# Performance work log

Measured on AMD Instinct MI355X. Metric: run time of the kernel, lower is better.

The kernel has to match this reference:

```python
import jax, jax.numpy as jnp
import numpy as np

B, T, I = 32768, 28, 28
H, C = 128, 10


def setup_inputs() -> dict:
    key = jax.random.key(0)
    ks = jax.random.split(key, 7)
    s_u = 1.0 / np.sqrt(I)
    s_w = 1.0 / np.sqrt(H)
    return {
        "x": jax.random.normal(ks[0], (B, T, I), dtype=jnp.float32),
        "U_w": jax.random.uniform(ks[1], (H, I), jnp.float32, -s_u, s_u),
        "U_b": jax.random.uniform(ks[2], (H,), jnp.float32, -s_u, s_u),
        "W_w": jax.random.uniform(ks[3], (H, H), jnp.float32, -s_w, s_w),
        "W_b": jax.random.uniform(ks[4], (H,), jnp.float32, -s_w, s_w),
        "V_w": jax.random.uniform(ks[5], (C, H), jnp.float32, -s_w, s_w),
        "V_b": jax.random.uniform(ks[6], (C,), jnp.float32, -s_w, s_w),
    }


def reference(x, U_w, U_b, W_w, W_b, V_w, V_b):
    # x: [B, T, I]. Precompute input projections for all timesteps at once
    # (one big GEMM), then scan the sequential recurrence on S.
    ux = jnp.einsum("bti,hi->tbh", x, U_w) + U_b  # [T, B, H]

    def step(S, ux_t):
        S = jnp.tanh(ux_t + S @ W_w.T + W_b)
        return S, None

    S0 = jnp.zeros((x.shape[0], W_w.shape[0]), dtype=x.dtype)
    S_final, _ = jax.lax.scan(step, S0, ux)
    return S_final @ V_w.T + V_b  # [B, C]
```

## Files before the change

### kernel.cpp

```cpp
#include <hip/hip_runtime.h>


#define T_STEPS 28
#define S_STRIDE 132
#define X_STRIDE 900
#define XSLOTS 3136

typedef __attribute__((ext_vector_type(4))) float f32x4;
typedef __attribute__((ext_vector_type(8))) short short8;

#define MFMA16 __builtin_amdgcn_mfma_f32_16x16x32_bf16

__device__ __forceinline__ unsigned pack2(float lo, float hi) {
#if __has_builtin(__builtin_amdgcn_cvt_pk_bf16_f32)
  auto p = __builtin_amdgcn_cvt_pk_bf16_f32(lo, hi);
  return __builtin_bit_cast(unsigned, p);
#else
  unsigned a = __builtin_bit_cast(unsigned, lo);
  a += 0x7FFFu + ((a >> 16) & 1u);
  unsigned b = __builtin_bit_cast(unsigned, hi);
  b += 0x7FFFu + ((b >> 16) & 1u);
  return (a >> 16) | (b & 0xFFFF0000u);
#endif
}

__device__ __forceinline__ float bf2f(unsigned short s) {
  return __builtin_bit_cast(float, (unsigned)s << 16);
}

__device__ __forceinline__ short8 to_frag(f32x4 a, f32x4 b) {
  union { unsigned u[4]; short8 v; } r;
  r.u[0] = pack2(a[0], a[1]);
  r.u[1] = pack2(a[2], a[3]);
  r.u[2] = pack2(b[0], b[1]);
  r.u[3] = pack2(b[2], b[3]);
  return r.v;
}

__device__ __forceinline__ short8 load_frag64(const unsigned short* sp, int off) {
  union { uint2 d[2]; short8 v; } r;
  r.d[0] = *(const uint2*)(sp + off);
  r.d[1] = *(const uint2*)(sp + off + 4);
  return r.v;
}

__device__ __forceinline__ f32x4 tanh4(f32x4 z) {
  f32x4 x2 = z * z;
  f32x4 p = 945.0f + x2 * (105.0f + x2);
  f32x4 q = 945.0f + x2 * (420.0f + 15.0f * x2);
  f32x4 num = z * p;
  f32x4 r;
#pragma unroll
  for (int i = 0; i < 4; ++i) r[i] = __builtin_amdgcn_rcpf(q[i]);
  f32x4 t = num * r;
#pragma unroll
  for (int i = 0; i < 4; ++i) t[i] = __builtin_amdgcn_fmed3f(t[i], -1.0f, 1.0f);
  return t;
}

__global__ __launch_bounds__(256, 4) void rnn_fused(
    const float* __restrict__ x,  const float* __restrict__ Uw,
    const float* __restrict__ Ub, const float* __restrict__ Ww,
    const float* __restrict__ Wb, const float* __restrict__ Vw,
    const float* __restrict__ Vb, float* __restrict__ out) {
  __shared__ __align__(16) unsigned short Sbuf[2][16 * S_STRIDE];
  __shared__ __align__(16) unsigned short Xbuf[16 * X_STRIDE];

  const int tid  = threadIdx.x;
  const int w    = tid >> 6;
  const int lane = tid & 63;
  const int l15  = lane & 15;
  const int q    = lane >> 4;
  const int mrow = w * 32;
  const int b0   = blockIdx.x * 16;

  const f32x4 zero4 = {0.f, 0.f, 0.f, 0.f};
  const float* xblk = x + (size_t)b0 * 784;

  {
    f32x4 xr[13];
#pragma unroll
    for (int k = 0; k < 13; ++k) {
      int s = tid + 256 * k;
      if (s < XSLOTS) xr[k] = *(const f32x4*)(xblk + s * 4);
    }
#pragma unroll
    for (int k = 0; k < 13; ++k) {
      int s = tid + 256 * k;
      if (s < XSLOTS) {
        int row = s / 196, g = s - row * 196, tt = g / 7, j = g - tt * 7;
        uint2 d; d.x = pack2(xr[k][0], xr[k][1]); d.y = pack2(xr[k][2], xr[k][3]);
        *(uint2*)(Xbuf + row * X_STRIDE + tt * 32 + j * 4) = d;
        if (j == 0) {
          uint2 zz; zz.x = 0u; zz.y = 0u;
          *(uint2*)(Xbuf + row * X_STRIDE + tt * 32 + 28) = zz;
        }
      }
    }
  }

  short8 wfrag[2][4];
  short8 ufrag[2];
  f32x4  bias[2];
#pragma unroll
  for (int mt = 0; mt < 2; ++mt) {
    const int h = mrow + mt * 16 + l15;
    const float* wp = Ww + h * 128 + q * 8;
#pragma unroll
    for (int kt = 0; kt < 4; ++kt) {
      wfrag[mt][kt] = to_frag(*(const f32x4*)wp, *(const f32x4*)(wp + 4));
      wp += 32;
    }
    const float* up = Uw + h * 28 + q * 8;
    f32x4 u0 = *(const f32x4*)up;
    f32x4 u1 = zero4;
    if (q < 3) u1 = *(const f32x4*)(up + 4);
    ufrag[mt] = to_frag(u0, u1);
    const int hb = mrow + mt * 16 + q * 4;
    bias[mt] = *(const f32x4*)(Wb + hb) + *(const f32x4*)(Ub + hb);
  }
  __syncthreads();

  const int ro = l15 * S_STRIDE;
  const int xo = l15 * X_STRIDE + q * 8;
  f32x4 acc[2];

  {
    short8 xf = load_frag64(&Xbuf[0], xo);
    unsigned short* wp = &Sbuf[1][0];
#pragma unroll
    for (int mt = 0; mt < 2; ++mt) {
      f32x4 d0 = MFMA16(ufrag[mt], xf, bias[mt], 0, 0, 0);
      f32x4 t0 = tanh4(d0);
      uint2 dd; dd.x = pack2(t0[0], t0[1]); dd.y = pack2(t0[2], t0[3]);
      *(uint2*)(wp + ro + mrow + mt * 16 + q * 4) = dd;
    }
  }
  __syncthreads();

#pragma unroll 1
  for (int t = 1; t < T_STEPS; ++t) {
    short8 xf = load_frag64(&Xbuf[0], xo + t * 32);

    const unsigned short* sp = &Sbuf[t & 1][0] + ro + q * 8;

    short8 sA = load_frag64(sp, 0);
#pragma unroll
    for (int mt = 0; mt < 2; ++mt)
      acc[mt] = MFMA16(wfrag[mt][0], sA, bias[mt], 0, 0, 0);
#pragma unroll
    for (int kt = 1; kt < 4; ++kt) {
      sA = load_frag64(sp, kt * 32);
#pragma unroll
      for (int mt = 0; mt < 2; ++mt)
        acc[mt] = MFMA16(wfrag[mt][kt], sA, acc[mt], 0, 0, 0);
    }
#pragma unroll
    for (int mt = 0; mt < 2; ++mt)
      acc[mt] = MFMA16(ufrag[mt], xf, acc[mt], 0, 0, 0);

    unsigned short* wp = &Sbuf[(t + 1) & 1][0];
#pragma unroll
    for (int mt = 0; mt < 2; ++mt) {
      f32x4 th = tanh4(acc[mt]);
      uint2 dd; dd.x = pack2(th[0], th[1]); dd.y = pack2(th[2], th[3]);
      *(uint2*)(wp + ro + mrow + mt * 16 + q * 4) = dd;
    }
    __syncthreads();
  }

  {
    const int r  = tid >> 4;
    const int c0 = tid & 15;
    if (c0 < 10) {
      const float* v0 = Vw + c0 * 128;
      const unsigned short* srow = &Sbuf[0][0] + r * S_STRIDE;
      float a0 = 0.f;
#pragma unroll 8
      for (int h = 0; h < 128; ++h) a0 += bf2f(srow[h]) * v0[h];
      out[(size_t)(b0 + r) * 10 + c0] = a0 + Vb[c0];
    }
  }
}

extern "C" void kernel_launch(void* const* d_in, const int* in_sizes, int n_in,
                              void* d_out, int out_size, void* d_ws, size_t ws_size,
                              hipStream_t stream) {
  const float* x  = (const float*)d_in[0];
  const float* Uw = (const float*)d_in[1];
  const float* Ub = (const float*)d_in[2];
  const float* Ww = (const float*)d_in[3];
  const float* Wb = (const float*)d_in[4];
  const float* Vw = (const float*)d_in[5];
  const float* Vb = (const float*)d_in[6];
  rnn_fused<<<2048, 256, 0, stream>>>(x, Uw, Ub, Ww, Wb, Vw, Vb, (float*)d_out);
}
```

Measured before the change: 202.9 us.

## Give each wavefront its own batch tile and drop block-wide barriers

Each wavefront now owns a 16-row batch tile and computes all 128 hidden units, holding the full W and U matrices as bf16 fragments in registers. This removes the per-step __syncthreads, because state exchange happens only within the wave through a private XOR-swizzled LDS double buffer. The x input is streamed from global memory one timestep ahead instead of being staged whole into LDS. The grid drops to 512 blocks and launch bounds are relaxed. The cost is far higher register pressure (32 W fragments per lane) and lower occupancy, with possible spills.

```diff
diff --git a/kernel.cpp b/kernel.cpp
--- a/kernel.cpp
+++ b/kernel.cpp
@@ -2,9 +2,6 @@
 
 
 #define T_STEPS 28
-#define S_STRIDE 132
-#define X_STRIDE 900
-#define XSLOTS 3136
 
 typedef __attribute__((ext_vector_type(4))) float f32x4;
 typedef __attribute__((ext_vector_type(8))) short short8;
@@ -24,23 +21,12 @@
 #endif
 }
 
-__device__ __forceinline__ float bf2f(unsigned short s) {
-  return __builtin_bit_cast(float, (unsigned)s << 16);
-}
-
 __device__ __forceinline__ short8 to_frag(f32x4 a, f32x4 b) {
   union { unsigned u[4]; short8 v; } r;
   r.u[0] = pack2(a[0], a[1]);
   r.u[1] = pack2(a[2], a[3]);
   r.u[2] = pack2(b[0], b[1]);
   r.u[3] = pack2(b[2], b[3]);
-  return r.v;
-}
-
-__device__ __forceinline__ short8 load_frag64(const unsigned short* sp, int off) {
-  union { uint2 d[2]; short8 v; } r;
-  r.d[0] = *(const uint2*)(sp + off);
-  r.d[1] = *(const uint2*)(sp + off + 4);
   return r.v;
 }
 
@@ -58,127 +44,119 @@
   return t;
 }
 
-__global__ __launch_bounds__(256, 4) void rnn_fused(
+__global__ __launch_bounds__(256) void rnn_fused(
     const float* __restrict__ x,  const float* __restrict__ Uw,
     const float* __restrict__ Ub, const float* __restrict__ Ww,
     const float* __restrict__ Wb, const float* __restrict__ Vw,
     const float* __restrict__ Vb, float* __restrict__ out) {
-  __shared__ __align__(16) unsigned short Sbuf[2][16 * S_STRIDE];
-  __shared__ __align__(16) unsigned short Xbuf[16 * X_STRIDE];
+  __shared__ __align__(16) char lds[4 * 2 * 16 * 256];
 
   const int tid  = threadIdx.x;
   const int w    = tid >> 6;
   const int lane = tid & 63;
   const int l15  = lane & 15;
   const int q    = lane >> 4;
-  const int mrow = w * 32;
-  const int b0   = blockIdx.x * 16;
+  const int bw   = (blockIdx.x * 4 + w) * 16;
 
+  char* WB       = lds + (w << 13);
+  const int rowb = l15 << 8;
+  const int swz  = (l15 & 7) << 4;
   const f32x4 zero4 = {0.f, 0.f, 0.f, 0.f};
-  const float* xblk = x + (size_t)b0 * 784;
+
+  const float* xp = x + (size_t)(bw + l15) * 784 + q * 8;
+
+  f32x4 xa = *(const f32x4*)xp;
+  f32x4 xb = zero4;
+  if (q < 3) xb = *(const f32x4*)(xp + 4);
+
+  short8 wfrag[8][4];
+  short8 ufrag[8];
+  f32x4  bias[8];
+#pragma unroll
+  for (int mt = 0; mt < 8; ++mt) {
+    const int h = mt * 16 + l15;
+    const float* wp = Ww + h * 128 + q * 8;
+#pragma unroll
+    for (int kt = 0; kt < 4; ++kt)
+      wfrag[mt][kt] =
+          to_frag(*(const f32x4*)(wp + kt * 32), *(const f32x4*)(wp + kt * 32 + 4));
+    const float* up = Uw + h * 28 + q * 8;
+    f32x4 u1 = zero4;
+    if (q < 3) u1 = *(const f32x4*)(up + 4);
+    ufrag[mt] = to_frag(*(const f32x4*)up, u1);
+    const int hb = mt * 16 + q * 4;
+    bias[mt] = *(const f32x4*)(Wb + hb) + *(const f32x4*)(Ub + hb);
+  }
 
   {
-    f32x4 xr[13];
+    short8 xf = to_frag(xa, xb);
+    const float* xn = xp + 28;
+    xa = *(const f32x4*)xn;
+    xb = zero4;
+    if (q < 3) xb = *(const f32x4*)(xn + 4);
 #pragma unroll
-    for (int k = 0; k < 13; ++k) {
-      int s = tid + 256 * k;
-      if (s < XSLOTS) xr[k] = *(const f32x4*)(xblk + s * 4);
+    for (int mt = 0; mt < 8; ++mt) {
+      f32x4 d  = MFMA16(ufrag[mt], xf, bias[mt], 0, 0, 0);
+      f32x4 th = tanh4(d);
+      uint2 dd; dd.x = pack2(th[0], th[1]); dd.y = pack2(th[2], th[3]);
+      *(uint2*)(WB + rowb + ((mt * 32 + q * 8) ^ swz)) = dd;
     }
+  }
+
+  const float* xn = xp + 56;
+#pragma unroll 1
+  for (int t = 1; t < T_STEPS; ++t) {
+    short8 xf = to_frag(xa, xb);
+    if (t < T_STEPS - 1) {
+      xa = *(const f32x4*)xn;
+      if (q < 3) xb = *(const f32x4*)(xn + 4); else xb = zero4;
+      xn += 28;
+    }
+    const char* rbuf = WB + (((t & 1) ^ 1) << 12);
+    char*       wbuf = WB + ((t & 1) << 12);
+
+    short8 sfrag[4];
 #pragma unroll
-    for (int k = 0; k < 13; ++k) {
-      int s = tid + 256 * k;
-      if (s < XSLOTS) {
-        int row = s / 196, g = s - row * 196, tt = g / 7, j = g - tt * 7;
-        uint2 d; d.x = pack2(xr[k][0], xr[k][1]); d.y = pack2(xr[k][2], xr[k][3]);
-        *(uint2*)(Xbuf + row * X_STRIDE + tt * 32 + j * 4) = d;
-        if (j == 0) {
-          uint2 zz; zz.x = 0u; zz.y = 0u;
-          *(uint2*)(Xbuf + row * X_STRIDE + tt * 32 + 28) = zz;
-        }
+    for (int kt = 0; kt < 4; ++kt)
+      sfrag[kt] = *(const short8*)(rbuf + rowb + ((kt * 64 + q * 16) ^ swz));
+
+#pragma unroll
+    for (int g = 0; g < 2; ++g) {
+      f32x4 acc[4];
+#pragma unroll
+      for (int i = 0; i < 4; ++i)
+        acc[i] = MFMA16(ufrag[g * 4 + i], xf, bias[g * 4 + i], 0, 0, 0);
+#pragma unroll
+      for (int kt = 0; kt < 4; ++kt)
+#pragma unroll
+        for (int i = 0; i < 4; ++i)
+          acc[i] = MFMA16(wfrag[g * 4 + i][kt], sfrag[kt], acc[i], 0, 0, 0);
+#pragma unroll
+      for (int i = 0; i < 4; ++i) {
+        f32x4 th = tanh4(acc[i]);
+        const int mt = g * 4 + i;
+        uint2 dd; dd.x = pack2(th[0], th[1]); dd.y = pack2(th[2], th[3]);
+        *(uint2*)(wbuf + rowb + ((mt * 32 + q * 8) ^ swz)) = dd;
       }
     }
   }
 
-  short8 wfrag[2][4];
-  short8 ufrag[2];
-  f32x4  bias[2];
+  {
+    const char* sb   = WB + (((T_STEPS - 1) & 1) << 12);
+    const int   br   = lane & 15;
+    const int   c0   = lane >> 4;
+    const char* srow = sb + (br << 8);
+    const int   sw   = (br & 7) << 4;
+    for (int c = c0; c < 10; c += 4) {
+      const float* vp = Vw + c * 128;
+      float a0 = Vb[c];
 #pragma unroll
-  for (int mt = 0; mt < 2; ++mt) {
-    const int h = mrow + mt * 16 + l15;
-    const float* wp = Ww + h * 128 + q * 8;
-#pragma unroll
-    for (int kt = 0; kt < 4; ++kt) {
-      wfrag[mt][kt] = to_frag(*(const f32x4*)wp, *(const f32x4*)(wp + 4));
-      wp += 32;
-    }
-    const float* up = Uw + h * 28 + q * 8;
-    f32x4 u0 = *(const f32x4*)up;
-    f32x4 u1 = zero4;
-    if (q < 3) u1 = *(const f32x4*)(up + 4);
-    ufrag[mt] = to_frag(u0, u1);
-    const int hb = mrow + mt * 16 + q * 4;
-    bias[mt] = *(const f32x4*)(Wb + hb) + *(const f32x4*)(Ub + hb);
-  }
-  __syncthreads();
-
-  const int ro = l15 * S_STRIDE;
-  const int xo = l15 * X_STRIDE + q * 8;
-  f32x4 acc[2];
-
-  {
-    short8 xf = load_frag64(&Xbuf[0], xo);
-    unsigned short* wp = &Sbuf[1][0];
-#pragma unroll
-    for (int mt = 0; mt < 2; ++mt) {
-      f32x4 d0 = MFMA16(ufrag[mt], xf, bias[mt], 0, 0, 0);
-      f32x4 t0 = tanh4(d0);
-      uint2 dd; dd.x = pack2(t0[0], t0[1]); dd.y = pack2(t0[2], t0[3]);
-      *(uint2*)(wp + ro + mrow + mt * 16 + q * 4) = dd;
-    }
-  }
-  __syncthreads();
-
-#pragma unroll 1
-  for (int t = 1; t < T_STEPS; ++t) {
-    short8 xf = load_frag64(&Xbuf[0], xo + t * 32);
-
-    const unsigned short* sp = &Sbuf[t & 1][0] + ro + q * 8;
-
-    short8 sA = load_frag64(sp, 0);
-#pragma unroll
-    for (int mt = 0; mt < 2; ++mt)
-      acc[mt] = MFMA16(wfrag[mt][0], sA, bias[mt], 0, 0, 0);
-#pragma unroll
-    for (int kt = 1; kt < 4; ++kt) {
-      sA = load_frag64(sp, kt * 32);
-#pragma unroll
-      for (int mt = 0; mt < 2; ++mt)
-        acc[mt] = MFMA16(wfrag[mt][kt], sA, acc[mt], 0, 0, 0);
-    }
-#pragma unroll
-    for (int mt = 0; mt < 2; ++mt)
-      acc[mt] = MFMA16(ufrag[mt], xf, acc[mt], 0, 0, 0);
-
-    unsigned short* wp = &Sbuf[(t + 1) & 1][0];
-#pragma unroll
-    for (int mt = 0; mt < 2; ++mt) {
-      f32x4 th = tanh4(acc[mt]);
-      uint2 dd; dd.x = pack2(th[0], th[1]); dd.y = pack2(th[2], th[3]);
-      *(uint2*)(wp + ro + mrow + mt * 16 + q * 4) = dd;
-    }
-    __syncthreads();
-  }
-
-  {
-    const int r  = tid >> 4;
-    const int c0 = tid & 15;
-    if (c0 < 10) {
-      const float* v0 = Vw + c0 * 128;
-      const unsigned short* srow = &Sbuf[0][0] + r * S_STRIDE;
-      float a0 = 0.f;
-#pragma unroll 8
-      for (int h = 0; h < 128; ++h) a0 += bf2f(srow[h]) * v0[h];
-      out[(size_t)(b0 + r) * 10 + c0] = a0 + Vb[c0];
+      for (int hh = 0; hh < 128; hh += 2) {
+        unsigned d = *(const unsigned*)(srow + ((hh * 2) ^ sw));
+        a0 += __builtin_bit_cast(float, d << 16) * vp[hh];
+        a0 += __builtin_bit_cast(float, d & 0xFFFF0000u) * vp[hh + 1];
+      }
+      out[(size_t)(bw + br) * 10 + c] = a0;
     }
   }
 }
@@ -193,5 +171,5 @@
   const float* Wb = (const float*)d_in[4];
   const float* Vw = (const float*)d_in[5];
   const float* Vb = (const float*)d_in[6];
-  rnn_fused<<<2048, 256, 0, stream>>>(x, Uw, Ub, Ww, Wb, Vw, Vb, (float*)d_out);
+  rnn_fused<<<512, 256, 0, stream>>>(x, Uw, Ub, Ww, Wb, Vw, Vb, (float*)d_out);
 }
```

After: 245.1 us. +20.8%, slower.

## Stream x per-timestep from global into registers instead of staging in LDS

Applied to the files above, without the earlier changes.

Drops the large LDS staging buffer for the whole x tile. Each lane now loads its own x fragment directly from global memory one timestep ahead, overlapping that load with the current step's MFMAs. Freeing about 29 KB of LDS per block permits higher occupancy, so launch bounds are raised from 4 to 6 blocks. The output projection is also vectorised with 8-byte and 16-byte loads. The risk is that global load latency becomes exposed inside the sequential loop, and the strided 112-byte row accesses are less coalesced.

```diff
diff --git a/kernel.cpp b/kernel.cpp
--- a/kernel.cpp
+++ b/kernel.cpp
@@ -3,8 +3,6 @@
 
 #define T_STEPS 28
 #define S_STRIDE 132
-#define X_STRIDE 900
-#define XSLOTS 3136
 
 typedef __attribute__((ext_vector_type(4))) float f32x4;
 typedef __attribute__((ext_vector_type(8))) short short8;
@@ -22,10 +20,6 @@
   b += 0x7FFFu + ((b >> 16) & 1u);
   return (a >> 16) | (b & 0xFFFF0000u);
 #endif
-}
-
-__device__ __forceinline__ float bf2f(unsigned short s) {
-  return __builtin_bit_cast(float, (unsigned)s << 16);
 }
 
 __device__ __forceinline__ short8 to_frag(f32x4 a, f32x4 b) {
@@ -58,13 +52,12 @@
   return t;
 }
 
-__global__ __launch_bounds__(256, 4) void rnn_fused(
+__global__ __launch_bounds__(256, 6) void rnn_fused(
     const float* __restrict__ x,  const float* __restrict__ Uw,
     const float* __restrict__ Ub, const float* __restrict__ Ww,
     const float* __restrict__ Wb, const float* __restrict__ Vw,
     const float* __restrict__ Vb, float* __restrict__ out) {
   __shared__ __align__(16) unsigned short Sbuf[2][16 * S_STRIDE];
-  __shared__ __align__(16) unsigned short Xbuf[16 * X_STRIDE];
 
   const int tid  = threadIdx.x;
   const int w    = tid >> 6;
@@ -75,29 +68,11 @@
   const int b0   = blockIdx.x * 16;
 
   const f32x4 zero4 = {0.f, 0.f, 0.f, 0.f};
-  const float* xblk = x + (size_t)b0 * 784;
 
-  {
-    f32x4 xr[13];
-#pragma unroll
-    for (int k = 0; k < 13; ++k) {
-      int s = tid + 256 * k;
-      if (s < XSLOTS) xr[k] = *(const f32x4*)(xblk + s * 4);
-    }
-#pragma unroll
-    for (int k = 0; k < 13; ++k) {
-      int s = tid + 256 * k;
-      if (s < XSLOTS) {
-        int row = s / 196, g = s - row * 196, tt = g / 7, j = g - tt * 7;
-        uint2 d; d.x = pack2(xr[k][0], xr[k][1]); d.y = pack2(xr[k][2], xr[k][3]);
-        *(uint2*)(Xbuf + row * X_STRIDE + tt * 32 + j * 4) = d;
-        if (j == 0) {
-          uint2 zz; zz.x = 0u; zz.y = 0u;
-          *(uint2*)(Xbuf + row * X_STRIDE + tt * 32 + 28) = zz;
-        }
-      }
-    }
-  }
+  const float* xp = x + (size_t)(b0 + l15) * 784 + q * 8;
+  f32x4 xa = *(const f32x4*)xp;
+  f32x4 xb = zero4;
+  if (q < 3) xb = *(const f32x4*)(xp + 4);
 
   short8 wfrag[2][4];
   short8 ufrag[2];
@@ -119,14 +94,14 @@
     const int hb = mrow + mt * 16 + q * 4;
     bias[mt] = *(const f32x4*)(Wb + hb) + *(const f32x4*)(Ub + hb);
   }
-  __syncthreads();
 
   const int ro = l15 * S_STRIDE;
-  const int xo = l15 * X_STRIDE + q * 8;
-  f32x4 acc[2];
 
   {
-    short8 xf = load_frag64(&Xbuf[0], xo);
+    short8 xf = to_frag(xa, xb);
+    const float* x1 = xp + 28;
+    xa = *(const f32x4*)x1;
+    if (q < 3) xb = *(const f32x4*)(x1 + 4);
     unsigned short* wp = &Sbuf[1][0];
 #pragma unroll
     for (int mt = 0; mt < 2; ++mt) {
@@ -138,9 +113,16 @@
   }
   __syncthreads();
 
+  const float* xn = xp + 56;
+  f32x4 acc[2];
 #pragma unroll 1
   for (int t = 1; t < T_STEPS; ++t) {
-    short8 xf = load_frag64(&Xbuf[0], xo + t * 32);
+    short8 xf = to_frag(xa, xb);
+    if (t < T_STEPS - 1) {
+      xa = *(const f32x4*)xn;
+      if (q < 3) xb = *(const f32x4*)(xn + 4);
+      xn += 28;
+    }
 
     const unsigned short* sp = &Sbuf[t & 1][0] + ro + q * 8;
 
@@ -173,12 +155,19 @@
     const int r  = tid >> 4;
     const int c0 = tid & 15;
     if (c0 < 10) {
-      const float* v0 = Vw + c0 * 128;
+      const float* vp = Vw + c0 * 128;
       const unsigned short* srow = &Sbuf[0][0] + r * S_STRIDE;
-      float a0 = 0.f;
-#pragma unroll 8
-      for (int h = 0; h < 128; ++h) a0 += bf2f(srow[h]) * v0[h];
-      out[(size_t)(b0 + r) * 10 + c0] = a0 + Vb[c0];
+      float a0 = Vb[c0];
+#pragma unroll
+      for (int h = 0; h < 128; h += 4) {
+        uint2 d  = *(const uint2*)(srow + h);
+        f32x4 v4 = *(const f32x4*)(vp + h);
+        a0 += __builtin_bit_cast(float, d.x << 16) * v4[0];
+        a0 += __builtin_bit_cast(float, d.x & 0xFFFF0000u) * v4[1];
+        a0 += __builtin_bit_cast(float, d.y << 16) * v4[2];
+        a0 += __builtin_bit_cast(float, d.y & 0xFFFF0000u) * v4[3];
+      }
+      out[(size_t)(b0 + r) * 10 + c0] = a0;
     }
   }
 }
```

After: 285.1 us. +40.5%, slower.
